# Performance work log

Hardware: AMD Instinct MI355X
Metric: run time of the kernel (lower is better)

The kernel has to match this reference:

```python
import jax, jax.numpy as jnp
import numpy as np

B, S, D, F, E, K = 4, 2048, 1024, 4096, 8, 1


def setup_inputs() -> dict:
    key = jax.random.key(0)
    ks = jax.random.split(key, 4)
    sc = lambda n: 1.0 / np.sqrt(n)
    return {
        "hidden_states": jax.random.normal(ks[0], (B, S, D), jnp.float32),
        "gate_w": jax.random.normal(ks[1], (E, D), jnp.float32) * sc(D),
        "w1": jax.random.normal(ks[2], (E, F, D), jnp.float32) * sc(D),
        "b1": jnp.zeros((E, F), jnp.float32),
        "w2": jax.random.normal(ks[3], (E, D, F), jnp.float32) * sc(F),
        "b2": jnp.zeros((E, D), jnp.float32),
    }


def moe_forward(hidden_states, gate_w, w1, b1, w2, b2, k=K):
    b, s, d = hidden_states.shape
    e = gate_w.shape[0]
    x = hidden_states.reshape(-1, d)  # [T, D]
    router_logits = x @ gate_w.T  # [T, E]
    router_probs = jax.nn.softmax(router_logits.astype(jnp.float32), axis=-1)
    topw, sel = jax.lax.top_k(router_probs, k)  # [T, k]
    topw = topw / topw.sum(axis=-1, keepdims=True)
    topw = topw.astype(x.dtype)

    # router z-loss: sum(logsumexp(logits)^2) / T
    log_z = jax.scipy.special.logsumexp(router_logits.astype(jnp.float32), axis=-1)
    z_loss = jnp.sum(log_z ** 2) / x.shape[0]

    # load balancing loss (torch code: one_hot(sel).max(-2) -> [T,E])
    router_prob_per_expert = jnp.mean(topw.astype(jnp.float32), axis=-2)  # [k]
    expert_mask = jax.nn.one_hot(sel, e, dtype=jnp.int32).max(axis=-2)  # [T, E]
    tokens_per_expert = jnp.mean(expert_mask.astype(jnp.float32), axis=-2)  # [E]
    aux_loss = jnp.mean(tokens_per_expert * router_prob_per_expert) * (e ** 2)

    # combine weights [T, E]: routing weight where expert selected, else 0
    combine = (jax.nn.one_hot(sel, e, dtype=x.dtype) * topw[..., None]).sum(axis=1)

    out = jnp.zeros_like(x)
    for ei in range(e):  # fixed small expert loop (structurally distinct params)
        h = jax.nn.gelu(x @ w1[ei].T + b1[ei])  # [T, F]
        y = h @ w2[ei].T + b2[ei]  # [T, D]
        out = out + combine[:, ei:ei + 1] * y
    return out.reshape(b, s, d), aux_loss, z_loss


def reference(hidden_states, gate_w, w1, b1, w2, b2):
    return moe_forward(hidden_states, gate_w, w1, b1, w2, b2)
```

## Files before the change

### kernel.cpp

```cpp
#include <hip/hip_runtime.h>
#include <hip/hip_bf16.h>
#include <stdint.h>

#define TOK 8192
#define DD 1024
#define FF 4096
#define EE 8
#define BM 256
#define BN 256
#define BK 64
#define NW 512
#define MT_MAX 40

typedef __attribute__((ext_vector_type(8))) short bf16x8;
typedef __attribute__((ext_vector_type(4))) float f32x4;

#define WS_SEL    0u
#define WS_CNT    32768u
#define WS_CUR    32832u
#define WS_TSTART 32896u
#define WS_ZSUM   32960u
#define WS_PERM   33024u
#define WS_XB     131072u
#define WS_H      (WS_XB + 16777216u)
#define WS_WB     (WS_H + 83886080u)

__device__ __forceinline__ unsigned short f2bf(float f) {
  unsigned int u = __builtin_bit_cast(unsigned int, f);
  u = (u + 0x7FFFu + ((u >> 16) & 1u)) >> 16;
  return (unsigned short)u;
}

__device__ __forceinline__ void async_copy16(const void* g, void* l) {
  __builtin_amdgcn_global_load_lds(
      (const __attribute__((address_space(1))) unsigned int*)g,
      (__attribute__((address_space(3))) unsigned int*)l, 16, 0, 0);
}

__global__ __launch_bounds__(256) void k_convert(const float* __restrict__ src,
                                                 unsigned short* __restrict__ dst,
                                                 int n4) {
  for (int i = (int)blockIdx.x * 256 + threadIdx.x; i < n4; i += (int)gridDim.x * 256) {
    const float4 v = ((const float4*)src)[i];
    ushort4 b;
    b.x = f2bf(v.x); b.y = f2bf(v.y); b.z = f2bf(v.z); b.w = f2bf(v.w);
    ((ushort4*)dst)[i] = b;
  }
}

__global__ __launch_bounds__(256) void k_router(const float* __restrict__ x,
                                                const float* __restrict__ gw,
                                                uint8_t* __restrict__ ws) {
  const int wv = threadIdx.x >> 6, l = threadIdx.x & 63;
  const int t = (int)blockIdx.x * 4 + wv;
  int* sel = (int*)(ws + WS_SEL);
  int* cnt = (int*)(ws + WS_CNT);
  float* zsum = (float*)(ws + WS_ZSUM);
  unsigned short* xb = (unsigned short*)(ws + WS_XB);
  const float4* xr = (const float4*)(x + (size_t)t * DD);
  double acc[EE];
#pragma unroll
  for (int e = 0; e < EE; ++e) acc[e] = 0.0;
#pragma unroll
  for (int i = 0; i < 4; ++i) {
    const int idx = l + i * 64;
    const float4 v = xr[idx];
    ushort4 b;
    b.x = f2bf(v.x); b.y = f2bf(v.y); b.z = f2bf(v.z); b.w = f2bf(v.w);
    *(ushort4*)(xb + (size_t)t * DD + (size_t)idx * 4) = b;
#pragma unroll
    for (int e = 0; e < EE; ++e) {
      const float4 g = ((const float4*)(gw + (size_t)e * DD))[idx];
      acc[e] += (double)v.x * g.x + (double)v.y * g.y +
                (double)v.z * g.z + (double)v.w * g.w;
    }
  }
#pragma unroll
  for (int e = 0; e < EE; ++e) {
#pragma unroll
    for (int s = 32; s > 0; s >>= 1) acc[e] += __shfl_xor(acc[e], s, 64);
  }
  if (l == 0) {
    double m = acc[0]; int am = 0;
#pragma unroll
    for (int e = 1; e < EE; ++e) if (acc[e] > m) { m = acc[e]; am = e; }
    float se = 0.f;
#pragma unroll
    for (int e = 0; e < EE; ++e) se += __expf((float)(acc[e] - m));
    const float lse = (float)m + __logf(se);
    sel[t] = am;
    atomicAdd(cnt + am, 1);
    atomicAdd(zsum, lse * lse);
  }
}

__global__ void k_finalize(uint8_t* __restrict__ ws, float* __restrict__ out) {
  if (threadIdx.x != 0 || blockIdx.x != 0) return;
  int* cnt = (int*)(ws + WS_CNT);
  int* cur = (int*)(ws + WS_CUR);
  int* ts = (int*)(ws + WS_TSTART);
  int tiles = 0, s = 0;
  for (int e = 0; e < EE; ++e) {
    ts[e] = tiles;
    cur[e] = tiles * BM;
    tiles += (cnt[e] + BM - 1) / BM;
    s += cnt[e];
  }
  ts[EE] = tiles;
  const float zs = *(float*)(ws + WS_ZSUM);
  out[(size_t)TOK * DD] = (float)EE * ((float)s / (float)TOK);
  out[(size_t)TOK * DD + 1] = zs / (float)TOK;
}

__global__ __launch_bounds__(256) void k_scatter(uint8_t* __restrict__ ws) {
  const int t = (int)blockIdx.x * 256 + threadIdx.x;
  if (t >= TOK) return;
  const int e = ((const int*)(ws + WS_SEL))[t];
  const int pos = atomicAdd((int*)(ws + WS_CUR) + e, 1);
  ((int*)(ws + WS_PERM))[pos] = t;
}

template <int K, int NTOT, int KSPLIT, bool DOGELU, bool INDIRECT>
__global__ __launch_bounds__(NW, 2) void k_gemm256(const unsigned short* __restrict__ A,
                                                   const unsigned short* __restrict__ W,
                                                   const float* __restrict__ bias,
                                                   uint8_t* __restrict__ ws,
                                                   float* __restrict__ out) {
  const int* ts = (const int*)(ws + WS_TSTART);
  const int* perm = (const int*)(ws + WS_PERM);
  unsigned short* H = (unsigned short*)(ws + WS_H);

  const int MT = (int)gridDim.x;
  const int NT = NTOT / BN;
  const int nblk = MT * (int)gridDim.y;
  const int orig = (int)blockIdx.y * MT + (int)blockIdx.x;
  const int q = nblk >> 3, r = nblk & 7;
  const int xcd = orig & 7, b8 = orig >> 3;
  const int wg = (xcd < r ? xcd * (q + 1) : r * (q + 1) + (xcd - r) * q) + b8;
  const int mt = wg % MT;
  const int rest = wg / MT;
  const int nt = rest % NT;
  const int kh = rest / NT;

  if (mt >= ts[EE]) return;
  int e = 0;
#pragma unroll
  for (int i = 1; i < EE; ++i) if (mt >= ts[i]) e = i;

  const int m0 = mt * BM, n0 = nt * BN;
  const unsigned short* We = W + (size_t)e * NTOT * K;
  const float* bs = bias + (size_t)e * NTOT;

  __shared__ __align__(16) unsigned short sm[2][2][BM * BK];

  const int tid = threadIdx.x, wid = tid >> 6, l = tid & 63;
  const int wr = wid >> 2, wc = wid & 3;

  f32x4 acc[8][4];
#pragma unroll
  for (int m = 0; m < 8; ++m)
#pragma unroll
    for (int n = 0; n < 4; ++n) acc[m][n] = f32x4{0.f, 0.f, 0.f, 0.f};

  int arow[4], brow[4];
#pragma unroll
  for (int j = 0; j < 4; ++j) {
    const int row = (tid + j * NW) >> 3;
    if (INDIRECT) {
      const int tk = perm[m0 + row];
      arow[j] = tk < 0 ? 0 : tk;
    } else {
      arow[j] = m0 + row;
    }
    brow[j] = n0 + row;
  }

  const int kbeg = kh * (K / KSPLIT);
  const int NS = (K / KSPLIT) / BK;

  auto stage = [&](int buf, int k0) {
#pragma unroll
    for (int j = 0; j < 4; ++j) {
      const int p = tid + j * NW;
      const int row = p >> 3, pc = p & 7;
      const int lc = pc ^ (row & 7);
      async_copy16(A + (size_t)arow[j] * K + k0 + lc * 8,
                   (char*)&sm[buf][0][0] + (size_t)p * 16);
      async_copy16(We + (size_t)brow[j] * K + k0 + lc * 8,
                   (char*)&sm[buf][1][0] + (size_t)p * 16);
    }
  };

  stage(0, kbeg);
  asm volatile("s_waitcnt vmcnt(0)" ::: "memory");
  __syncthreads();

  int cur = 0;
  for (int t = 0; t < NS; ++t) {
    if (t + 1 < NS) stage(cur ^ 1, kbeg + (t + 1) * BK);
    const char* Ab = (const char*)&sm[cur][0][0];
    const char* Bb = (const char*)&sm[cur][1][0];
#pragma unroll
    for (int kk = 0; kk < 2; ++kk) {
      const int ch = kk * 4 + (l >> 4);
      bf16x8 af[8], bf_[4];
#pragma unroll
      for (int m = 0; m < 8; ++m) {
        const int row = wr * 128 + m * 16 + (l & 15);
        af[m] = *(const bf16x8*)(Ab + row * 128 + ((ch ^ (row & 7)) << 4));
      }
#pragma unroll
      for (int n = 0; n < 4; ++n) {
        const int row = wc * 64 + n * 16 + (l & 15);
        bf_[n] = *(const bf16x8*)(Bb + row * 128 + ((ch ^ (row & 7)) << 4));
      }
#pragma unroll
      for (int m = 0; m < 8; ++m)
#pragma unroll
        for (int n = 0; n < 4; ++n)
          acc[m][n] = __builtin_amdgcn_mfma_f32_16x16x32_bf16(af[m], bf_[n], acc[m][n], 0, 0, 0);
    }
    asm volatile("s_waitcnt vmcnt(0)" ::: "memory");
    __syncthreads();
    cur ^= 1;
  }

  const int cl = l & 15, rg = l >> 4;
#pragma unroll
  for (int n = 0; n < 4; ++n) {
    const int col = n0 + wc * 64 + n * 16 + cl;
    const float bv = (KSPLIT == 1 || kh == 0) ? bs[col] : 0.f;
#pragma unroll
    for (int m = 0; m < 8; ++m) {
      const int rbase = m0 + wr * 128 + m * 16 + rg * 4;
#pragma unroll
      for (int qq = 0; qq < 4; ++qq) {
        const int rr = rbase + qq;
        float v = acc[m][n][qq] + bv;
        if (DOGELU) {
          const float u0 = 0.7978845608028654f * (v + 0.044715f * v * v * v);
          const float th = 1.f - 2.f / (__expf(2.f * u0) + 1.f);
          v = 0.5f * v * (1.f + th);
          H[(size_t)rr * FF + col] = f2bf(v);
        } else {
          const int tk = perm[rr];
          if (tk >= 0) {
            if (KSPLIT == 1) out[(size_t)tk * DD + col] = v;
            else atomicAdd(out + (size_t)tk * DD + col, v);
          }
        }
      }
    }
  }
}

extern "C" void kernel_launch(void* const* d_in, const int* in_sizes, int n_in,
                              void* d_out, int out_size, void* d_ws, size_t ws_size,
                              hipStream_t stream) {
  const float* x = (const float*)d_in[0];
  const float* gw = (const float*)d_in[1];
  const float* w1 = (const float*)d_in[2];
  const float* b1 = (const float*)d_in[3];
  const float* w2 = (const float*)d_in[4];
  const float* b2 = (const float*)d_in[5];
  float* out = (float*)d_out;
  uint8_t* ws = (uint8_t*)d_ws;

  hipMemsetAsync(ws + WS_CNT, 0, 256, stream);
  hipMemsetAsync(ws + WS_PERM, 0xFF, MT_MAX * BM * 4, stream);
  hipMemsetAsync(out, 0, (size_t)TOK * DD * 4, stream);

  unsigned short* wb = (unsigned short*)(ws + WS_WB);
  const unsigned short* Xb = (const unsigned short*)(ws + WS_XB);
  const unsigned short* Hb = (const unsigned short*)(ws + WS_H);

  k_convert<<<2048, 256, 0, stream>>>(w1, wb, EE * FF * DD / 4);
  k_router<<<TOK / 4, 256, 0, stream>>>(x, gw, ws);
  k_finalize<<<1, 64, 0, stream>>>(ws, out);
  k_scatter<<<TOK / 256, 256, 0, stream>>>(ws);

  k_gemm256<DD, FF, 1, true, true>
      <<<dim3(MT_MAX, FF / BN), NW, 0, stream>>>(Xb, wb, b1, ws, out);

  k_convert<<<2048, 256, 0, stream>>>(w2, wb, EE * DD * FF / 4);

  k_gemm256<FF, DD, 4, false, false>
      <<<dim3(MT_MAX, (DD / BN) * 4), NW, 0, stream>>>(Hb, wb, b2, ws, out);
}
```

Measured before the change: 824.5 us.

## Deepen GEMM pipeline to four LDS stages with BK=32 and halve K-split

The GEMM K-tile shrinks from 64 to 32 and the LDS buffers go from a double buffer to a 4-stage ring with three tiles prefetched. Waits use partial vmcnt counts and raw s_barrier, so a thread waits only for the oldest tile instead of draining all outstanding loads each step. The LDS swizzle is reworked for the 64-byte rows. Separately, the second GEMM's K-split drops from 4 to 2, which cuts atomic/partial-sum traffic but also halves the number of workgroups. The risks are more barriers per unit of K, and the raw s_barrier without a full LDS fence may race when a ring slot is refilled.

```diff
diff --git a/kernel.cpp b/kernel.cpp
--- a/kernel.cpp
+++ b/kernel.cpp
@@ -8,7 +8,7 @@
 #define EE 8
 #define BM 256
 #define BN 256
-#define BK 64
+#define BK 32
 #define NW 512
 #define MT_MAX 40
 
@@ -151,7 +151,7 @@
   const unsigned short* We = W + (size_t)e * NTOT * K;
   const float* bs = bias + (size_t)e * NTOT;
 
-  __shared__ __align__(16) unsigned short sm[2][2][BM * BK];
+  __shared__ __align__(16) unsigned short sm[4][2][BM * BK];
 
   const int tid = threadIdx.x, wid = tid >> 6, l = tid & 63;
   const int wr = wid >> 2, wc = wid & 3;
@@ -162,10 +162,10 @@
 #pragma unroll
     for (int n = 0; n < 4; ++n) acc[m][n] = f32x4{0.f, 0.f, 0.f, 0.f};
 
-  int arow[4], brow[4];
-#pragma unroll
-  for (int j = 0; j < 4; ++j) {
-    const int row = (tid + j * NW) >> 3;
+  int arow[2], brow[2];
+#pragma unroll
+  for (int j = 0; j < 2; ++j) {
+    const int row = (tid + j * NW) >> 2;
     if (INDIRECT) {
       const int tk = perm[m0 + row];
       arow[j] = tk < 0 ? 0 : tk;
@@ -180,10 +180,10 @@
 
   auto stage = [&](int buf, int k0) {
 #pragma unroll
-    for (int j = 0; j < 4; ++j) {
+    for (int j = 0; j < 2; ++j) {
       const int p = tid + j * NW;
-      const int row = p >> 3, pc = p & 7;
-      const int lc = pc ^ (row & 7);
+      const int row = p >> 2, pc = p & 3;
+      const int lc = pc ^ (row & 3) ^ ((row >> 2) & 3);
       async_copy16(A + (size_t)arow[j] * K + k0 + lc * 8,
                    (char*)&sm[buf][0][0] + (size_t)p * 16);
       async_copy16(We + (size_t)brow[j] * K + k0 + lc * 8,
@@ -192,37 +192,42 @@
   };
 
   stage(0, kbeg);
-  asm volatile("s_waitcnt vmcnt(0)" ::: "memory");
-  __syncthreads();
-
-  int cur = 0;
+  stage(1, kbeg + BK);
+  stage(2, kbeg + 2 * BK);
+  asm volatile("s_waitcnt vmcnt(8)" ::: "memory");
+  __builtin_amdgcn_s_barrier();
+  __builtin_amdgcn_sched_barrier(0);
+
+  const int ch = l >> 4;
   for (int t = 0; t < NS; ++t) {
-    if (t + 1 < NS) stage(cur ^ 1, kbeg + (t + 1) * BK);
-    const char* Ab = (const char*)&sm[cur][0][0];
-    const char* Bb = (const char*)&sm[cur][1][0];
-#pragma unroll
-    for (int kk = 0; kk < 2; ++kk) {
-      const int ch = kk * 4 + (l >> 4);
-      bf16x8 af[8], bf_[4];
-#pragma unroll
-      for (int m = 0; m < 8; ++m) {
-        const int row = wr * 128 + m * 16 + (l & 15);
-        af[m] = *(const bf16x8*)(Ab + row * 128 + ((ch ^ (row & 7)) << 4));
-      }
-#pragma unroll
-      for (int n = 0; n < 4; ++n) {
-        const int row = wc * 64 + n * 16 + (l & 15);
-        bf_[n] = *(const bf16x8*)(Bb + row * 128 + ((ch ^ (row & 7)) << 4));
-      }
-#pragma unroll
-      for (int m = 0; m < 8; ++m)
-#pragma unroll
-        for (int n = 0; n < 4; ++n)
-          acc[m][n] = __builtin_amdgcn_mfma_f32_16x16x32_bf16(af[m], bf_[n], acc[m][n], 0, 0, 0);
-    }
-    asm volatile("s_waitcnt vmcnt(0)" ::: "memory");
-    __syncthreads();
-    cur ^= 1;
+    const char* Ab = (const char*)&sm[t & 3][0][0];
+    const char* Bb = (const char*)&sm[t & 3][1][0];
+    bf16x8 af[8], bf_[4];
+#pragma unroll
+    for (int m = 0; m < 8; ++m) {
+      const int row = wr * 128 + m * 16 + (l & 15);
+      const int s = ch ^ (row & 3) ^ ((row >> 2) & 3);
+      af[m] = *(const bf16x8*)(Ab + row * 64 + s * 16);
+    }
+#pragma unroll
+    for (int n = 0; n < 4; ++n) {
+      const int row = wc * 64 + n * 16 + (l & 15);
+      const int s = ch ^ (row & 3) ^ ((row >> 2) & 3);
+      bf_[n] = *(const bf16x8*)(Bb + row * 64 + s * 16);
+    }
+    if (t + 3 < NS) stage((t + 3) & 3, kbeg + (t + 3) * BK);
+#pragma unroll
+    for (int m = 0; m < 8; ++m)
+#pragma unroll
+      for (int n = 0; n < 4; ++n)
+        acc[m][n] = __builtin_amdgcn_mfma_f32_16x16x32_bf16(af[m], bf_[n], acc[m][n], 0, 0, 0);
+    if (t + 1 < NS) {
+      if (t + 3 < NS)       asm volatile("s_waitcnt vmcnt(8)" ::: "memory");
+      else if (t + 3 == NS) asm volatile("s_waitcnt vmcnt(4)" ::: "memory");
+      else                  asm volatile("s_waitcnt vmcnt(0)" ::: "memory");
+      __builtin_amdgcn_s_barrier();
+      __builtin_amdgcn_sched_barrier(0);
+    }
   }
 
   const int cl = l & 15, rg = l >> 4;
@@ -284,6 +289,6 @@
 
   k_convert<<<2048, 256, 0, stream>>>(w2, wb, EE * DD * FF / 4);
 
-  k_gemm256<FF, DD, 4, false, false>
-      <<<dim3(MT_MAX, (DD / BN) * 4), NW, 0, stream>>>(Hb, wb, b2, ws, out);
-}
+  k_gemm256<FF, DD, 2, false, false>
+      <<<dim3(MT_MAX, (DD / BN) * 2), NW, 0, stream>>>(Hb, wb, b2, ws, out);
+}
```

Result: faster. 801.5 us (-2.8%).
